# Optimization experiments

Hardware: AMD Instinct MI355X
Metric: run time of the kernel (lower is better)

Reference implementation:

```python
import jax, jax.numpy as jnp
import numpy as np

N = 500000
D = 128
B = 16384

def setup_inputs() -> dict:
    key = jax.random.key(0)
    k1, k2, k3, k4 = jax.random.split(key, 4)
    x = jax.random.normal(k1, (N, D), dtype=jnp.float32)
    ref = jax.random.normal(k2, (N, D), dtype=jnp.float32)
    index = jnp.sort(jax.random.randint(k3, (N,), 0, B))
    W = jax.random.normal(k4, (2 * D, 1), dtype=jnp.float32) * (1.0 / np.sqrt(2 * D))
    b = jnp.zeros((1,), dtype=jnp.float32)
    return {"x": x, "ref": ref, "index": index, "batch_size": B, "W": W, "b": b}

def reference(x, ref, index, batch_size, W, b):
    # src: [N, 1] attention logits
    src = jnp.tanh(jnp.concatenate([x, ref], axis=-1) @ W + b)
    # segment softmax (max is detached in the original via .detach())
    seg_max = jax.ops.segment_max(jax.lax.stop_gradient(src), index,
                                  num_segments=batch_size)
    out = jnp.exp(src - seg_max[index])
    out_sum = jax.ops.segment_sum(out, index, num_segments=batch_size) + 1e-16
    w = out / out_sum[index]            # [N, 1] normalized weights
    # weighted sum of x per segment -> [batch_size, D]
    return jax.ops.segment_sum(w * x, index, num_segments=batch_size)
```

## Files before the change

### kernel.cpp

```cpp
#include <hip/hip_runtime.h>
#include <math.h>

#define D 128

__global__ __launch_bounds__(256) void attn_seg_kernel(
    const float* __restrict__ x,
    const float* __restrict__ ref,
    const int*   __restrict__ index,
    const float* __restrict__ W,
    const float* __restrict__ b,
    float*       __restrict__ out,
    int N)
{
    const int seg  = blockIdx.x;
    const int tid  = threadIdx.x;
    const int wave = tid >> 6;
    const int lane = tid & 63;

    int lo = 0, hi = N;
    while (lo < hi) { int mid = (lo + hi) >> 1; if (index[mid] < seg) lo = mid + 1; else hi = mid; }
    const int start = lo;
    hi = N;
    while (lo < hi) { int mid = (lo + hi) >> 1; if (index[mid] < seg + 1) lo = mid + 1; else hi = mid; }
    const int end = lo;

    const float2 wx = ((const float2*)W)[lane];
    const float2 wr = ((const float2*)(W + D))[lane];
    const float bias = b[0];

    float2 acc = make_float2(0.f, 0.f);
    float  sum_e = 0.f;

    for (int r = start + wave; r < end; r += 4) {
        const size_t row = (size_t)r * D;
        const float2 xv = ((const float2*)(x   + row))[lane];
        const float2 rv = ((const float2*)(ref + row))[lane];
        float partial = xv.x * wx.x + xv.y * wx.y + rv.x * wr.x + rv.y * wr.y;
        #pragma unroll
        for (int off = 32; off >= 1; off >>= 1)
            partial += __shfl_xor(partial, off);
        const float src = tanhf(partial + bias);
        const float e   = __expf(src);
        acc.x += e * xv.x;
        acc.y += e * xv.y;
        sum_e += e;
    }

    __shared__ float lds_acc[4][D];
    __shared__ float lds_sum[4];
    ((float2*)lds_acc[wave])[lane] = acc;
    if (lane == 0) lds_sum[wave] = sum_e;
    __syncthreads();

    if (tid < D) {
        const float t = lds_acc[0][tid] + lds_acc[1][tid] + lds_acc[2][tid] + lds_acc[3][tid];
        const float s = lds_sum[0] + lds_sum[1] + lds_sum[2] + lds_sum[3] + 1e-16f;
        out[(size_t)seg * D + tid] = t / s;
    }
}

extern "C" void kernel_launch(void* const* d_in, const int* in_sizes, int n_in,
                              void* d_out, int out_size, void* d_ws, size_t ws_size,
                              hipStream_t stream) {
    const float* x     = (const float*)d_in[0];
    const float* ref   = (const float*)d_in[1];
    const int*   index = (const int*)d_in[2];
    const float* W     = (const float*)d_in[4];
    const float* b     = (const float*)d_in[5];
    float* out = (float*)d_out;

    const int N = in_sizes[0] / D;
    const int B = out_size / D;

    attn_seg_kernel<<<B, 256, 0, stream>>>(x, ref, index, W, b, out, N);
}
```

Measured before the change: 521.8 us.

## Precompute segment starts, use float4 half-wave rows with prefetch and fast tanh

Adds a pre-pass kernel that writes segment start offsets into the workspace, replacing two binary searches per block. The main kernel now has each half-wave handle one row with float4 loads, so 8 rows are in flight per block. It software-prefetches the next row into registers and replaces tanhf with an exp/rcp formulation. The cost is an extra kernel launch, one more pass over the index array, and somewhat lower accuracy in tanh.

```diff
diff --git a/kernel.cpp b/kernel.cpp
--- a/kernel.cpp
+++ b/kernel.cpp
@@ -3,58 +3,107 @@
 
 #define D 128
 
+__global__ __launch_bounds__(256) void seg_starts_kernel(
+    const int* __restrict__ index, int* __restrict__ starts, int N, int B)
+{
+    int i = blockIdx.x * blockDim.x + threadIdx.x;
+    if (i >= N) return;
+    int cur  = index[i];
+    int prev = (i == 0) ? -1 : index[i - 1];
+    for (int j = prev + 1; j <= cur; ++j) starts[j] = i;
+    if (i == N - 1) {
+        for (int j = cur + 1; j <= B; ++j) starts[j] = N;
+    }
+}
+
+__device__ __forceinline__ float fast_exp_tanh(float v) {
+    float e2 = __expf(2.0f * v);
+    float th = 1.0f - 2.0f * __builtin_amdgcn_rcpf(1.0f + e2);
+    return __expf(th);
+}
+
 __global__ __launch_bounds__(256) void attn_seg_kernel(
     const float* __restrict__ x,
     const float* __restrict__ ref,
-    const int*   __restrict__ index,
+    const int*   __restrict__ starts,
     const float* __restrict__ W,
     const float* __restrict__ b,
-    float*       __restrict__ out,
-    int N)
+    float*       __restrict__ out)
 {
     const int seg  = blockIdx.x;
     const int tid  = threadIdx.x;
     const int wave = tid >> 6;
     const int lane = tid & 63;
+    const int hl   = lane >> 5;
+    const int c    = lane & 31;
 
-    int lo = 0, hi = N;
-    while (lo < hi) { int mid = (lo + hi) >> 1; if (index[mid] < seg) lo = mid + 1; else hi = mid; }
-    const int start = lo;
-    hi = N;
-    while (lo < hi) { int mid = (lo + hi) >> 1; if (index[mid] < seg + 1) lo = mid + 1; else hi = mid; }
-    const int end = lo;
+    const int start = starts[seg];
+    const int end   = starts[seg + 1];
+    const int cnt   = end - start;
 
-    const float2 wx = ((const float2*)W)[lane];
-    const float2 wr = ((const float2*)(W + D))[lane];
+    const float4 wx = ((const float4*)W)[c];
+    const float4 wr = ((const float4*)(W + D))[c];
     const float bias = b[0];
 
-    float2 acc = make_float2(0.f, 0.f);
+    float4 acc   = make_float4(0.f, 0.f, 0.f, 0.f);
     float  sum_e = 0.f;
 
-    for (int r = start + wave; r < end; r += 4) {
-        const size_t row = (size_t)r * D;
-        const float2 xv = ((const float2*)(x   + row))[lane];
-        const float2 rv = ((const float2*)(ref + row))[lane];
-        float partial = xv.x * wx.x + xv.y * wx.y + rv.x * wr.x + rv.y * wr.y;
+    const int niter = (cnt + 7) >> 3;
+    const int rbase = start + (wave << 1) + hl;
+
+    if (niter > 0) {
+        const int last = end - 1;
+        int cur_r = rbase;
+        int row   = min(cur_r, last);
+        float4 xv = ((const float4*)(x   + (size_t)row * D))[c];
+        float4 rv = ((const float4*)(ref + (size_t)row * D))[c];
+
+        for (int it = 1; it < niter; ++it) {
+            const int nxt_r = rbase + (it << 3);
+            const int nrow  = min(nxt_r, last);
+            float4 xn = ((const float4*)(x   + (size_t)nrow * D))[c];
+            float4 rn = ((const float4*)(ref + (size_t)nrow * D))[c];
+
+            float partial = xv.x*wx.x + xv.y*wx.y + xv.z*wx.z + xv.w*wx.w
+                          + rv.x*wr.x + rv.y*wr.y + rv.z*wr.z + rv.w*wr.w;
+            #pragma unroll
+            for (int off = 16; off >= 1; off >>= 1)
+                partial += __shfl_xor(partial, off);
+            float e = fast_exp_tanh(partial + bias);
+            e = (cur_r < end) ? e : 0.f;
+            acc.x += e * xv.x; acc.y += e * xv.y;
+            acc.z += e * xv.z; acc.w += e * xv.w;
+            sum_e += e;
+
+            xv = xn; rv = rn; cur_r = nxt_r;
+        }
+
+        float partial = xv.x*wx.x + xv.y*wx.y + xv.z*wx.z + xv.w*wx.w
+                      + rv.x*wr.x + rv.y*wr.y + rv.z*wr.z + rv.w*wr.w;
         #pragma unroll
-        for (int off = 32; off >= 1; off >>= 1)
+        for (int off = 16; off >= 1; off >>= 1)
             partial += __shfl_xor(partial, off);
-        const float src = tanhf(partial + bias);
-        const float e   = __expf(src);
-        acc.x += e * xv.x;
-        acc.y += e * xv.y;
+        float e = fast_exp_tanh(partial + bias);
+        e = (cur_r < end) ? e : 0.f;
+        acc.x += e * xv.x; acc.y += e * xv.y;
+        acc.z += e * xv.z; acc.w += e * xv.w;
         sum_e += e;
     }
 
-    __shared__ float lds_acc[4][D];
-    __shared__ float lds_sum[4];
-    ((float2*)lds_acc[wave])[lane] = acc;
-    if (lane == 0) lds_sum[wave] = sum_e;
+    __shared__ float lds_acc[8][D];
+    __shared__ float lds_sum[8];
+    const int half_id = (wave << 1) | hl;
+    ((float4*)lds_acc[half_id])[c] = acc;
+    if (c == 0) lds_sum[half_id] = sum_e;
     __syncthreads();
 
     if (tid < D) {
-        const float t = lds_acc[0][tid] + lds_acc[1][tid] + lds_acc[2][tid] + lds_acc[3][tid];
-        const float s = lds_sum[0] + lds_sum[1] + lds_sum[2] + lds_sum[3] + 1e-16f;
+        float t = 0.f;
+        float s = 1e-16f;
+        #pragma unroll
+        for (int k = 0; k < 8; ++k) t += lds_acc[k][tid];
+        #pragma unroll
+        for (int k = 0; k < 8; ++k) s += lds_sum[k];
         out[(size_t)seg * D + tid] = t / s;
     }
 }
@@ -72,5 +121,8 @@
     const int N = in_sizes[0] / D;
     const int B = out_size / D;
 
-    attn_seg_kernel<<<B, 256, 0, stream>>>(x, ref, index, W, b, out, N);
+    int* starts = (int*)d_ws;
+
+    seg_starts_kernel<<<(N + 255) / 256, 256, 0, stream>>>(index, starts, N, B);
+    attn_seg_kernel<<<B, 256, 0, stream>>>(x, ref, starts, W, b, out);
 }
```

Result: faster. 495.9 us (-5.0%).
